# Optimization experiments

Hardware: AMD Instinct MI355X
Metric: run time of the kernel (lower is better)

The kernel has to match this reference:

```python
import jax, jax.numpy as jnp
import numpy as np

GAMMA = 0.95        # gamma_lemma: persistence decay per cycle (eq. 12.1)
KAPPA = 0.1         # kappa_interfere: lateral interference strength (eq. 12.3)
T_STEPS = 50        # t_lemma_steps: integration window before selection (eq. 12.2)
FLOOR = 1e-6        # confidence_floor for peak-to-average ratio

B, N_CONCEPTS, N_LEMMAS = 4096, 1024, 512


def setup_inputs() -> dict:
    key = jax.random.key(0)
    k1, k2 = jax.random.split(key, 2)
    # kernel boundary hands in a normalized concept distribution
    c_raw = jax.random.uniform(k1, (B, N_CONCEPTS), dtype=jnp.float32)
    c_lex = c_raw / jnp.sum(c_raw, axis=-1, keepdims=True)
    # TiedSubstrate W_C_to_L: (out_dim=n_lemmas, in_dim=n_concepts)
    W = jax.random.normal(k2, (N_LEMMAS, N_CONCEPTS), dtype=jnp.float32) / np.sqrt(N_CONCEPTS)
    # persistent lemma activation buffer a_lemma, zero at reset
    a0 = jnp.zeros((B, N_LEMMAS), dtype=jnp.float32)
    return {"c_lex": c_lex, "W": W, "a0": a0}


def reference(c_lex, W, a0):
    """Integrate lemma activations for T_STEPS cycles, then select.

    Per cycle (eq. 12.1 + 12.3):
      a <- gamma * a + c_lex @ W^T            # decay + concept->lemma drive
      a <- a - kappa * (sum_j a_j - a)        # lateral interference from other lemmas
      a <- max(a, 0)                          # rectify activations
    Selection (eq. 12.2): argmax over lemmas; confidence = peak / max(mean, floor).
    """
    def step(a, _):
        a = GAMMA * a + jnp.einsum('bc,lc->bl', c_lex, W)   # (B, n_lemmas)
        a = a - KAPPA * (jnp.sum(a, axis=-1, keepdims=True) - a)
        a = jnp.maximum(a, 0.0)
        return a, None

    a, _ = jax.lax.scan(step, a0, None, length=T_STEPS)
    peak = jnp.max(a, axis=-1)
    mean = jnp.mean(a, axis=-1)
    confidence = peak / jnp.maximum(mean, FLOOR)
    selected = jnp.argmax(a, axis=-1)
    return a, selected, confidence
```

## Files before the change

### kernel.cpp

```cpp
#include <hip/hip_runtime.h>
#include <hip/hip_bf16.h>

#define BATCH 4096
#define NC    1024
#define NL    512
#define TSTEPS 50
#define GAMMA_C 0.95f
#define KAPPA_C 0.1f
#define FLOOR_C 1e-6f

typedef __attribute__((ext_vector_type(8))) short short8;
typedef __attribute__((ext_vector_type(4))) float f32x4;

__device__ inline void split_bf16(float x, unsigned short& h, unsigned short& l) {
    unsigned u = __float_as_uint(x);
    unsigned rh = u + 0x7FFFu + ((u >> 16) & 1u);
    h = (unsigned short)(rh >> 16);
    float hf = __uint_as_float((unsigned)h << 16);
    float r = x - hf;
    unsigned v = __float_as_uint(r);
    unsigned rl = v + 0x7FFFu + ((v >> 16) & 1u);
    l = (unsigned short)(rl >> 16);
}

__global__ __launch_bounds__(256)
void convert_w(const float* __restrict__ W,
               unsigned short* __restrict__ Whi, unsigned short* __restrict__ Wlo) {
    const int fidx = (blockIdx.x * 256 + threadIdx.x) * 4;
    const float4 v = *(const float4*)(W + fidx);
    ushort4 h4, l4;
    split_bf16(v.x, h4.x, l4.x);
    split_bf16(v.y, h4.y, l4.y);
    split_bf16(v.z, h4.z, l4.z);
    split_bf16(v.w, h4.w, l4.w);
    *(ushort4*)(Whi + fidx) = h4;
    *(ushort4*)(Wlo + fidx) = l4;
}

#define TM 128
#define TN 256
#define GK 32
#define LDT 40

__global__ __launch_bounds__(512)
void gemm_bf16x2(const float* __restrict__ A,
                 const unsigned short* __restrict__ Whi, const unsigned short* __restrict__ Wlo,
                 float* __restrict__ Dp, int kPerSplit) {
    __shared__ unsigned short AsH[TM * LDT];
    __shared__ unsigned short AsL[TM * LDT];
    __shared__ unsigned short BsH[TN * LDT];
    __shared__ unsigned short BsL[TN * LDT];

    const int tid = threadIdx.x;
    const int m0 = blockIdx.x * TM;
    const int n0 = blockIdx.y * TN;
    const int kb = blockIdx.z * kPerSplit;

    const int srA = tid >> 2;
    const int kcA = (tid & 3) * 8;
    const int srB = tid >> 1;
    const int kcB = (tid & 1) * 16;

    const float*          gA  = A   + (size_t)(m0 + srA) * NC + kb + kcA;
    const unsigned short* gBh = Whi + (size_t)(n0 + srB) * NC + kb + kcB;
    const unsigned short* gBl = Wlo + (size_t)(n0 + srB) * NC + kb + kcB;

    unsigned short* wAh = AsH + srA * LDT + kcA;
    unsigned short* wAl = AsL + srA * LDT + kcA;
    unsigned short* wBh = BsH + srB * LDT + kcB;
    unsigned short* wBl = BsL + srB * LDT + kcB;

    const int lane = tid & 63;
    const int w    = tid >> 6;
    const int mw   = (w >> 2) * 64;
    const int nw   = (w & 3) * 64;
    const int sr   = lane & 15;
    const int quad = lane >> 4;

    const unsigned short* rAh = AsH + (mw + sr) * LDT + quad * 8;
    const unsigned short* rAl = AsL + (mw + sr) * LDT + quad * 8;
    const unsigned short* rBh = BsH + (nw + sr) * LDT + quad * 8;
    const unsigned short* rBl = BsL + (nw + sr) * LDT + quad * 8;

    f32x4 acc[4][4];
    #pragma unroll
    for (int i = 0; i < 4; ++i)
        #pragma unroll
        for (int j = 0; j < 4; ++j)
            acc[i][j] = (f32x4){0.f, 0.f, 0.f, 0.f};

    float4 pA0 = *(const float4*)gA;
    float4 pA1 = *(const float4*)(gA + 4);
    short8 pBh0 = *(const short8*)gBh;
    short8 pBh1 = *(const short8*)(gBh + 8);
    short8 pBl0 = *(const short8*)gBl;
    short8 pBl1 = *(const short8*)(gBl + 8);

    for (int kt = 0; kt < kPerSplit; kt += GK) {
        {
            short8 h8, l8;
            const float av[8] = {pA0.x, pA0.y, pA0.z, pA0.w, pA1.x, pA1.y, pA1.z, pA1.w};
            #pragma unroll
            for (int i = 0; i < 8; ++i) {
                unsigned short h, l;
                split_bf16(av[i], h, l);
                h8[i] = (short)h; l8[i] = (short)l;
            }
            *(short8*)wAh = h8;
            *(short8*)wAl = l8;
        }
        *(short8*)wBh = pBh0;
        *(short8*)(wBh + 8) = pBh1;
        *(short8*)wBl = pBl0;
        *(short8*)(wBl + 8) = pBl1;
        __syncthreads();

        const int kn = (kt + GK < kPerSplit) ? kt + GK : 0;
        pA0 = *(const float4*)(gA + kn);
        pA1 = *(const float4*)(gA + kn + 4);
        pBh0 = *(const short8*)(gBh + kn);
        pBh1 = *(const short8*)(gBh + kn + 8);
        pBl0 = *(const short8*)(gBl + kn);
        pBl1 = *(const short8*)(gBl + kn + 8);

        short8 afh[4], afl[4], bfh[4], bfl[4];
        #pragma unroll
        for (int mi = 0; mi < 4; ++mi) {
            afh[mi] = *(const short8*)(rAh + mi * 16 * LDT);
            afl[mi] = *(const short8*)(rAl + mi * 16 * LDT);
        }
        #pragma unroll
        for (int ni = 0; ni < 4; ++ni) {
            bfh[ni] = *(const short8*)(rBh + ni * 16 * LDT);
            bfl[ni] = *(const short8*)(rBl + ni * 16 * LDT);
        }

        #pragma unroll
        for (int mi = 0; mi < 4; ++mi) {
            #pragma unroll
            for (int ni = 0; ni < 4; ++ni) {
                acc[mi][ni] = __builtin_amdgcn_mfma_f32_16x16x32_bf16(
                    afh[mi], bfh[ni], acc[mi][ni], 0, 0, 0);
                acc[mi][ni] = __builtin_amdgcn_mfma_f32_16x16x32_bf16(
                    afh[mi], bfl[ni], acc[mi][ni], 0, 0, 0);
                acc[mi][ni] = __builtin_amdgcn_mfma_f32_16x16x32_bf16(
                    afl[mi], bfh[ni], acc[mi][ni], 0, 0, 0);
            }
        }
        __syncthreads();
    }

    float* Dz = Dp + (size_t)blockIdx.z * BATCH * NL;
    #pragma unroll
    for (int mi = 0; mi < 4; ++mi) {
        #pragma unroll
        for (int ni = 0; ni < 4; ++ni) {
            const int col = n0 + nw + ni * 16 + sr;
            #pragma unroll
            for (int r = 0; r < 4; ++r) {
                const int row = m0 + mw + mi * 16 + quad * 4 + r;
                Dz[(size_t)row * NL + col] = acc[mi][ni][r];
            }
        }
    }
}

template<int SK>
__global__ __launch_bounds__(256)
void iterate_select(const float* __restrict__ Dp,
                    float* __restrict__ a_out,
                    float* __restrict__ sel_out, float* __restrict__ conf_out) {
    const int lane = threadIdx.x & 63;
    const int wave = threadIdx.x >> 6;
    const int row  = blockIdx.x * 4 + wave;

    float d[8];
    {
        const float4* p0 = (const float4*)(Dp + (size_t)row * NL + lane * 8);
        float4 v0 = p0[0], v1 = p0[1];
        d[0] = v0.x; d[1] = v0.y; d[2] = v0.z; d[3] = v0.w;
        d[4] = v1.x; d[5] = v1.y; d[6] = v1.z; d[7] = v1.w;
        #pragma unroll
        for (int s = 1; s < SK; ++s) {
            const float4* ps = (const float4*)(Dp + (size_t)s * BATCH * NL
                                               + (size_t)row * NL + lane * 8);
            const float4 w0 = ps[0], w1 = ps[1];
            d[0] += w0.x; d[1] += w0.y; d[2] += w0.z; d[3] += w0.w;
            d[4] += w1.x; d[5] += w1.y; d[6] += w1.z; d[7] += w1.w;
        }
    }

    float a[8];
    #pragma unroll
    for (int j = 0; j < 8; ++j) a[j] = 0.f;

    const float K1 = 1.0f + KAPPA_C;

    for (int t = 0; t < TSTEPS; ++t) {
        #pragma unroll
        for (int j = 0; j < 8; ++j) a[j] = fmaf(GAMMA_C, a[j], d[j]);

        float t4a = a[0] + a[4], t4b = a[1] + a[5], t4c = a[2] + a[6], t4d = a[3] + a[7];
        float t2a = t4a + t4c, t2b = t4b + t4d;
        float S = t2a + t2b;

        S += __shfl_xor(S, 1, 64);
        S += __shfl_xor(S, 2, 64);
        S += __shfl_xor(S, 4, 64);
        S += __shfl_xor(S, 8, 64);
        S += __shfl_xor(S, 16, 64);
        S += __shfl_xor(S, 32, 64);

        const float h = -KAPPA_C * S;
        #pragma unroll
        for (int j = 0; j < 8; ++j) {
            const float v = fmaf(K1, a[j], h);
            a[j] = v > 0.f ? v : 0.f;
        }
    }

    float m4a = fmaxf(a[0], a[4]), m4b = fmaxf(a[1], a[5]);
    float m4c = fmaxf(a[2], a[6]), m4d = fmaxf(a[3], a[7]);
    float peak = fmaxf(fmaxf(m4a, m4b), fmaxf(m4c, m4d));
    float s4a = a[0] + a[4], s4b = a[1] + a[5], s4c = a[2] + a[6], s4d = a[3] + a[7];
    float ssum = (s4a + s4b) + (s4c + s4d);

    #pragma unroll
    for (int m = 1; m < 64; m <<= 1) {
        peak = fmaxf(peak, __shfl_xor(peak, m, 64));
        ssum += __shfl_xor(ssum, m, 64);
    }

    const float mean = ssum * (1.0f / (float)NL);
    const float conf = peak / fmaxf(mean, FLOOR_C);

    int idx = 0x7fffffff;
    #pragma unroll
    for (int j = 0; j < 8; ++j)
        if (a[j] == peak) idx = min(idx, lane * 8 + j);
    #pragma unroll
    for (int m = 1; m < 64; m <<= 1)
        idx = min(idx, __shfl_xor(idx, m, 64));

    float4* ar = (float4*)(a_out + (size_t)row * NL + lane * 8);
    float4 o0, o1;
    o0.x = a[0]; o0.y = a[1]; o0.z = a[2]; o0.w = a[3];
    o1.x = a[4]; o1.y = a[5]; o1.z = a[6]; o1.w = a[7];
    ar[0] = o0; ar[1] = o1;

    if (lane == 0) {
        if (sel_out)  sel_out[row]  = (float)idx;
        if (conf_out) conf_out[row] = conf;
    }
}

extern "C" void kernel_launch(void* const* d_in, const int* in_sizes, int n_in,
                              void* d_out, int out_size, void* d_ws, size_t ws_size,
                              hipStream_t stream) {
    const float* c_lex = (const float*)d_in[0];
    const float* W     = (const float*)d_in[1];

    float* D = (float*)d_ws;
    unsigned short* Whi = (unsigned short*)(D + 4ull * BATCH * NL);
    unsigned short* Wlo = Whi + (size_t)NL * NC;

    float* a_out = (float*)d_out;
    float* sel   = nullptr;
    float* conf  = nullptr;
    const int base = BATCH * NL;
    if (out_size >= base + 2 * BATCH) {
        sel  = a_out + base;
        conf = a_out + base + BATCH;
    } else if (out_size >= base + BATCH) {
        conf = a_out + base;
    }

    convert_w<<<dim3(512), 256, 0, stream>>>(W, Whi, Wlo);

    const int kPerSplit = NC / 4;
    gemm_bf16x2<<<dim3(BATCH / TM, NL / TN, 4), 512, 0, stream>>>(
        c_lex, Whi, Wlo, D, kPerSplit);

    iterate_select<4><<<dim3(BATCH / 4), 256, 0, stream>>>(D, a_out, sel, conf);
}
```

Baseline: 113.4 us.

## Pre-split activations to bf16 and load GEMM tiles via global_load_lds

Activations are now split into bf16 hi/lo halves in a separate conversion pass together with W, so the GEMM streams ready bf16 data with direct global-to-LDS loads instead of register staging and in-loop conversion. The tile shrinks to 128x128 with 256 threads, the unpadded LDS layout is used, and split-K drops from 4 to 2, halving the partial-sum buffer. In exchange, the hi/lo activation arrays must be written to and re-read from global memory. The new loop also loses the register prefetch overlap and may hit LDS bank conflicts because the rows are no longer padded.

```diff
diff --git a/kernel.cpp b/kernel.cpp
--- a/kernel.cpp
+++ b/kernel.cpp
@@ -24,63 +24,69 @@
 }
 
 __global__ __launch_bounds__(256)
-void convert_w(const float* __restrict__ W,
-               unsigned short* __restrict__ Whi, unsigned short* __restrict__ Wlo) {
-    const int fidx = (blockIdx.x * 256 + threadIdx.x) * 4;
-    const float4 v = *(const float4*)(W + fidx);
+void convert_split(const float* __restrict__ A, const float* __restrict__ W,
+                   unsigned short* __restrict__ Ahi, unsigned short* __restrict__ Alo,
+                   unsigned short* __restrict__ Whi, unsigned short* __restrict__ Wlo) {
+    const int chunk = blockIdx.x * 256 + threadIdx.x;
+    const int fidx  = chunk * 4;
+    const float* src;
+    unsigned short *dh, *dl;
+    if (fidx < BATCH * NC) {
+        src = A + fidx; dh = Ahi + fidx; dl = Alo + fidx;
+    } else {
+        const int o = fidx - BATCH * NC;
+        src = W + o; dh = Whi + o; dl = Wlo + o;
+    }
+    const float4 v = *(const float4*)src;
     ushort4 h4, l4;
     split_bf16(v.x, h4.x, l4.x);
     split_bf16(v.y, h4.y, l4.y);
     split_bf16(v.z, h4.z, l4.z);
     split_bf16(v.w, h4.w, l4.w);
-    *(ushort4*)(Whi + fidx) = h4;
-    *(ushort4*)(Wlo + fidx) = l4;
+    *(ushort4*)dh = h4;
+    *(ushort4*)dl = l4;
+}
+
+__device__ __forceinline__ void gld_lds16(const void* g, void* l) {
+    __builtin_amdgcn_global_load_lds(
+        (const __attribute__((address_space(1))) unsigned int*)g,
+        (__attribute__((address_space(3))) unsigned int*)l,
+        16, 0, 0);
 }
 
 #define TM 128
-#define TN 256
+#define TN 128
 #define GK 32
-#define LDT 40
-
-__global__ __launch_bounds__(512)
-void gemm_bf16x2(const float* __restrict__ A,
+
+__global__ __launch_bounds__(256)
+void gemm_bf16x2(const unsigned short* __restrict__ Ahi, const unsigned short* __restrict__ Alo,
                  const unsigned short* __restrict__ Whi, const unsigned short* __restrict__ Wlo,
                  float* __restrict__ Dp, int kPerSplit) {
-    __shared__ unsigned short AsH[TM * LDT];
-    __shared__ unsigned short AsL[TM * LDT];
-    __shared__ unsigned short BsH[TN * LDT];
-    __shared__ unsigned short BsL[TN * LDT];
+    __shared__ unsigned short AsH[TM * GK];
+    __shared__ unsigned short AsL[TM * GK];
+    __shared__ unsigned short BsH[TN * GK];
+    __shared__ unsigned short BsL[TN * GK];
 
     const int tid = threadIdx.x;
     const int m0 = blockIdx.x * TM;
     const int n0 = blockIdx.y * TN;
     const int kb = blockIdx.z * kPerSplit;
 
-    const int srA = tid >> 2;
-    const int kcA = (tid & 3) * 8;
-    const int srB = tid >> 1;
-    const int kcB = (tid & 1) * 16;
-
-    const float*          gA  = A   + (size_t)(m0 + srA) * NC + kb + kcA;
-    const unsigned short* gBh = Whi + (size_t)(n0 + srB) * NC + kb + kcB;
-    const unsigned short* gBl = Wlo + (size_t)(n0 + srB) * NC + kb + kcB;
-
-    unsigned short* wAh = AsH + srA * LDT + kcA;
-    unsigned short* wAl = AsL + srA * LDT + kcA;
-    unsigned short* wBh = BsH + srB * LDT + kcB;
-    unsigned short* wBl = BsL + srB * LDT + kcB;
-
     const int lane = tid & 63;
     const int w    = tid >> 6;
-    const int mw   = (w >> 2) * 64;
-    const int nw   = (w & 3) * 64;
+
+    const int lr = lane >> 2;
+    const int lk = (lane & 3) * 8;
+
+    const int mw   = (w >> 1) * 64;
+    const int nw   = (w & 1) * 64;
     const int sr   = lane & 15;
     const int quad = lane >> 4;
 
-    const unsigned short* rAh = AsH + (mw + sr) * LDT + quad * 8;
-    const unsigned short* rAl = AsL + (mw + sr) * LDT + quad * 8;
-    const unsigned short* rBh = BsH + (nw + sr) * LDT + quad * 8;
-    const unsigned short* rBl = BsL + (nw + sr) * LDT + quad * 8;
+    const unsigned short* rAh = AsH + (mw + sr) * GK + quad * 8;
+    const unsigned short* rAl = AsL + (mw + sr) * GK + quad * 8;
+    const unsigned short* rBh = BsH + (nw + sr) * GK + quad * 8;
+    const unsigned short* rBl = BsL + (nw + sr) * GK + quad * 8;
 
     f32x4 acc[4][4];
     #pragma unroll
@@ -89,50 +95,31 @@
         for (int j = 0; j < 4; ++j)
             acc[i][j] = (f32x4){0.f, 0.f, 0.f, 0.f};
 
-    float4 pA0 = *(const float4*)gA;
-    float4 pA1 = *(const float4*)(gA + 4);
-    short8 pBh0 = *(const short8*)gBh;
-    short8 pBh1 = *(const short8*)(gBh + 8);
-    short8 pBl0 = *(const short8*)gBl;
-    short8 pBl1 = *(const short8*)(gBl + 8);
-
     for (int kt = 0; kt < kPerSplit; kt += GK) {
-        {
-            short8 h8, l8;
-            const float av[8] = {pA0.x, pA0.y, pA0.z, pA0.w, pA1.x, pA1.y, pA1.z, pA1.w};
-            #pragma unroll
-            for (int i = 0; i < 8; ++i) {
-                unsigned short h, l;
-                split_bf16(av[i], h, l);
-                h8[i] = (short)h; l8[i] = (short)l;
-            }
-            *(short8*)wAh = h8;
-            *(short8*)wAl = l8;
-        }
-        *(short8*)wBh = pBh0;
-        *(short8*)(wBh + 8) = pBh1;
-        *(short8*)wBl = pBl0;
-        *(short8*)(wBl + 8) = pBl1;
         __syncthreads();
-
-        const int kn = (kt + GK < kPerSplit) ? kt + GK : 0;
-        pA0 = *(const float4*)(gA + kn);
-        pA1 = *(const float4*)(gA + kn + 4);
-        pBh0 = *(const short8*)(gBh + kn);
-        pBh1 = *(const short8*)(gBh + kn + 8);
-        pBl0 = *(const short8*)(gBl + kn);
-        pBl1 = *(const short8*)(gBl + kn + 8);
+        const size_t ko = (size_t)(kb + kt);
+        #pragma unroll
+        for (int j = 0; j < 2; ++j) {
+            const int i16 = w * 2 + j;
+            const size_t ga = (size_t)(m0 + i16 * 16 + lr) * NC + ko + lk;
+            const size_t gb = (size_t)(n0 + i16 * 16 + lr) * NC + ko + lk;
+            gld_lds16(Ahi + ga, AsH + i16 * 512);
+            gld_lds16(Alo + ga, AsL + i16 * 512);
+            gld_lds16(Whi + gb, BsH + i16 * 512);
+            gld_lds16(Wlo + gb, BsL + i16 * 512);
+        }
+        __syncthreads();
 
         short8 afh[4], afl[4], bfh[4], bfl[4];
         #pragma unroll
         for (int mi = 0; mi < 4; ++mi) {
-            afh[mi] = *(const short8*)(rAh + mi * 16 * LDT);
-            afl[mi] = *(const short8*)(rAl + mi * 16 * LDT);
+            afh[mi] = *(const short8*)(rAh + mi * 16 * GK);
+            afl[mi] = *(const short8*)(rAl + mi * 16 * GK);
         }
         #pragma unroll
         for (int ni = 0; ni < 4; ++ni) {
-            bfh[ni] = *(const short8*)(rBh + ni * 16 * LDT);
-            bfl[ni] = *(const short8*)(rBl + ni * 16 * LDT);
+            bfh[ni] = *(const short8*)(rBh + ni * 16 * GK);
+            bfl[ni] = *(const short8*)(rBl + ni * 16 * GK);
         }
 
         #pragma unroll
@@ -147,7 +134,6 @@
                     afl[mi], bfh[ni], acc[mi][ni], 0, 0, 0);
             }
         }
-        __syncthreads();
     }
 
     float* Dz = Dp + (size_t)blockIdx.z * BATCH * NL;
@@ -261,7 +247,9 @@
     const float* W     = (const float*)d_in[1];
 
     float* D = (float*)d_ws;
-    unsigned short* Whi = (unsigned short*)(D + 4ull * BATCH * NL);
+    unsigned short* Ahi = (unsigned short*)(D + 2ull * BATCH * NL);
+    unsigned short* Alo = Ahi + (size_t)BATCH * NC;
+    unsigned short* Whi = Alo + (size_t)BATCH * NC;
     unsigned short* Wlo = Whi + (size_t)NL * NC;
 
     float* a_out = (float*)d_out;
@@ -275,11 +263,11 @@
         conf = a_out + base;
     }
 
-    convert_w<<<dim3(512), 256, 0, stream>>>(W, Whi, Wlo);
-
-    const int kPerSplit = NC / 4;
-    gemm_bf16x2<<<dim3(BATCH / TM, NL / TN, 4), 512, 0, stream>>>(
-        c_lex, Whi, Wlo, D, kPerSplit);
-
-    iterate_select<4><<<dim3(BATCH / 4), 256, 0, stream>>>(D, a_out, sel, conf);
-}
+    convert_split<<<dim3(4608), 256, 0, stream>>>(c_lex, W, Ahi, Alo, Whi, Wlo);
+
+    const int kPerSplit = NC / 2;
+    gemm_bf16x2<<<dim3(BATCH / TM, NL / TN, 2), 256, 0, stream>>>(
+        Ahi, Alo, Whi, Wlo, D, kPerSplit);
+
+    iterate_select<2><<<dim3(BATCH / 4), 256, 0, stream>>>(D, a_out, sel, conf);
+}
```

Result: slower. 117.9 us (+3.9%).
